# Performance work log

Measured on AMD Instinct MI355X. Metric: run time of the kernel, lower is better.

Reference implementation:

```python
import jax, jax.numpy as jnp
import numpy as np

B, T, C = 2, 2048, 1024
N_HEAD = 16
HEAD_DIM = C // N_HEAD


def setup_inputs() -> dict:
    key = jax.random.key(0)
    k1, k2, k3 = jax.random.split(key, 3)
    s = 1.0 / np.sqrt(C)
    return {
        "x": jax.random.normal(k1, (B, T, C), dtype=jnp.float32),
        "w_qkv": jax.random.normal(k2, (C, 3 * C), dtype=jnp.float32) * s,
        "b_qkv": jnp.zeros((3 * C,), dtype=jnp.float32),
        "w_out": jax.random.normal(k3, (C, C), dtype=jnp.float32) * s,
        "b_out": jnp.zeros((C,), dtype=jnp.float32),
    }


def reference(x, w_qkv, b_qkv, w_out, b_out):
    b, t, c = x.shape
    qkv = x @ w_qkv + b_qkv                                   # [B,T,3C]
    # Faithful to torch: view(B,T,H,3*hd).transpose(1,2) then split last dim
    qkv = qkv.reshape(b, t, N_HEAD, 3 * HEAD_DIM).transpose(0, 2, 1, 3)  # [B,H,T,3hd]
    q, k, v = jnp.split(qkv, 3, axis=-1)                      # each [B,H,T,hd]
    att = jnp.einsum("bhqd,bhkd->bhqk", q, k) / np.sqrt(HEAD_DIM)
    causal = jnp.tril(jnp.ones((t, t), dtype=bool))
    att = jnp.where(causal[None, None], att, -jnp.inf)
    att = jax.nn.softmax(att, axis=-1)                        # dropout p=0 (eval)
    y = jnp.einsum("bhqk,bhkd->bhqd", att, v)                 # [B,H,T,hd]
    y = y.transpose(0, 2, 1, 3).reshape(b, t, c)
    return y @ w_out + b_out
```

## Files before the change

kernel.cpp:

```cpp
#include <hip/hip_runtime.h>


#define T_SEQ 2048
#define C_DIM 1024
#define NH    16
#define HD    64
#define BT    4096

typedef short bf16x8 __attribute__((ext_vector_type(8)));
typedef float floatx4 __attribute__((ext_vector_type(4)));

static __device__ __forceinline__ unsigned short f2bf(float f) {
    union { float f; unsigned u; } v; v.f = f;
    unsigned u = v.u;
    return (unsigned short)((u + 0x7FFFu + ((u >> 16) & 1u)) >> 16);
}
static __device__ __forceinline__ float bf2f(unsigned short u) {
    union { unsigned u; float f; } v; v.u = ((unsigned)u) << 16; return v.f;
}
static __device__ __forceinline__ float exp2_fast(float x) {
    float r; asm("v_exp_f32 %0, %1" : "=v"(r) : "v"(x)); return r;
}
static __device__ __forceinline__ unsigned cvt_pk_bf16(float lo, float hi) {
    unsigned r; asm("v_cvt_pk_bf16_f32 %0, %1, %2" : "=v"(r) : "v"(lo), "v"(hi)); return r;
}

static __device__ __forceinline__ void gl2lds16(const void* g, void* l) {
    __builtin_amdgcn_global_load_lds(
        (const __attribute__((address_space(1))) unsigned int*)g,
        (__attribute__((address_space(3))) unsigned int*)l, 16, 0, 0);
}

static __device__ __forceinline__ void transpose_body(float (*tile)[65],
                                                      const float* __restrict__ W,
                                                      unsigned short* __restrict__ Wt,
                                                      int K, int N, int bx, int by) {
    const int k0 = by << 6;
    const int n0 = bx << 6;
    const int rr = threadIdx.x >> 4;
    const int cc = (threadIdx.x & 15) << 2;
#pragma unroll
    for (int i = 0; i < 4; i++) {
        int r = rr + (i << 4);
        *(float4*)&tile[r][cc] = *(const float4*)(W + (size_t)(k0 + r) * N + n0 + cc);
    }
    __syncthreads();
#pragma unroll
    for (int i = 0; i < 4; i++) {
        int nr = rr + (i << 4);
        ushort4 o;
        o.x = f2bf(tile[cc + 0][nr]);
        o.y = f2bf(tile[cc + 1][nr]);
        o.z = f2bf(tile[cc + 2][nr]);
        o.w = f2bf(tile[cc + 3][nr]);
        *(ushort4*)(Wt + (size_t)(n0 + nr) * K + k0 + cc) = o;
    }
}

__global__ __launch_bounds__(256) void prep(const float* __restrict__ x,
                                            unsigned short* __restrict__ xb,
                                            const float* __restrict__ w_qkv,
                                            unsigned short* __restrict__ wqkvT,
                                            const float* __restrict__ w_out,
                                            unsigned short* __restrict__ woutT) {
    __shared__ float tile[64][65];
    const int bx = blockIdx.x;
    if (bx < 1024) {
        int i = (bx * 256 + threadIdx.x) * 4;
        const int n = BT * C_DIM;
        const int stride = 1024 * 1024;
        for (; i < n; i += stride) {
            float4 f = *(const float4*)(x + i);
            ushort4 o;
            o.x = f2bf(f.x); o.y = f2bf(f.y); o.z = f2bf(f.z); o.w = f2bf(f.w);
            *(ushort4*)(xb + i) = o;
        }
    } else if (bx < 1024 + 768) {
        int b = bx - 1024;
        transpose_body(tile, w_qkv, wqkvT, 1024, 3072, b % 48, b / 48);
    } else {
        int b = bx - 1024 - 768;
        transpose_body(tile, w_out, woutT, 1024, 1024, b % 16, b / 16);
    }
}

__global__ __launch_bounds__(256) void transp_v(const unsigned short* __restrict__ vb,
                                                unsigned short* __restrict__ vt) {
    __shared__ unsigned short tile[64][68];
    const int t0 = blockIdx.x << 6;
    const int bh = blockIdx.y;
    const size_t base = (size_t)bh * T_SEQ * HD;
    const int r = threadIdx.x >> 3;
    const int c = (threadIdx.x & 7) << 3;
#pragma unroll
    for (int i = 0; i < 2; i++) {
        const unsigned short* src = vb + base + (size_t)(t0 + r + (i << 5)) * HD + c;
        ushort4 u0 = *(const ushort4*)src;
        ushort4 u1 = *(const ushort4*)(src + 4);
        *(ushort4*)&tile[r + (i << 5)][c] = u0;
        *(ushort4*)&tile[r + (i << 5)][c + 4] = u1;
    }
    __syncthreads();
#pragma unroll
    for (int i = 0; i < 2; i++) {
        int s = threadIdx.x + (i << 8);
        int d = s >> 3;
        int tc = (s & 7) << 3;
        ushort4 o0, o1;
        o0.x = tile[tc + 0][d]; o0.y = tile[tc + 1][d];
        o0.z = tile[tc + 2][d]; o0.w = tile[tc + 3][d];
        o1.x = tile[tc + 4][d]; o1.y = tile[tc + 5][d];
        o1.z = tile[tc + 6][d]; o1.w = tile[tc + 7][d];
        unsigned short* dst = vt + ((size_t)bh * HD + d) * T_SEQ + t0 + tc;
        *(ushort4*)dst = o0;
        *(ushort4*)(dst + 4) = o1;
    }
}

#define GEMM_CORE(A_, Bt_, K_)                                                      \
    __shared__ short As[128 * 64];                                                  \
    __shared__ short Bs[128 * 64];                                                  \
    const int tid  = threadIdx.x;                                                   \
    const int lane = tid & 63, wave = tid >> 6;                                     \
    const int ln   = lane & 15, quad = lane >> 4;                                   \
    const int wm   = wave & 1,  wn   = wave >> 1;                                   \
    const int row0 = blockIdx.y << 7;                                               \
    const int col0 = blockIdx.x << 7;                                               \
    floatx4 acc[4][4];                                                              \
    _Pragma("unroll")                                                               \
    for (int i = 0; i < 4; i++)                                                     \
        _Pragma("unroll")                                                           \
        for (int j = 0; j < 4; j++) acc[i][j] = (floatx4){0.f, 0.f, 0.f, 0.f};      \
    for (int k0 = 0; k0 < K_; k0 += 64) {                                           \
        _Pragma("unroll")                                                           \
        for (int i = 0; i < 4; i++) {                                               \
            int c = (i << 8) + tid;                                                 \
            int r = c >> 3;                                                         \
            int gsrc = (c & 7) ^ (r & 7);                                           \
            gl2lds16(A_  + (size_t)(row0 + r) * K_ + k0 + (gsrc << 3), &As[c << 3]); \
            gl2lds16(Bt_ + (size_t)(col0 + r) * K_ + k0 + (gsrc << 3), &Bs[c << 3]); \
        }                                                                           \
        __syncthreads();                                                            \
        _Pragma("unroll")                                                           \
        for (int half = 0; half < 2; half++) {                                      \
            bf16x8 af[4], bfr[4];                                                   \
            _Pragma("unroll")                                                       \
            for (int t4 = 0; t4 < 4; t4++) {                                        \
                int ra = (wm << 6) + (t4 << 4) + ln;                                \
                int rb = (wn << 6) + (t4 << 4) + ln;                                \
                int g  = (half << 2) + quad;                                        \
                af[t4]  = *(bf16x8*)&As[((ra << 3) + (g ^ (ra & 7))) << 3];         \
                bfr[t4] = *(bf16x8*)&Bs[((rb << 3) + (g ^ (rb & 7))) << 3];         \
            }                                                                       \
            _Pragma("unroll")                                                       \
            for (int mt = 0; mt < 4; mt++)                                          \
                _Pragma("unroll")                                                   \
                for (int nt = 0; nt < 4; nt++)                                      \
                    acc[mt][nt] = __builtin_amdgcn_mfma_f32_16x16x32_bf16(af[mt], bfr[nt], acc[mt][nt], 0, 0, 0); \
        }                                                                           \
        __syncthreads();                                                            \
    }

__global__ __launch_bounds__(256) void gemm_qkv(const unsigned short* __restrict__ A,
                                                const unsigned short* __restrict__ Bt,
                                                const float* __restrict__ bias,
                                                unsigned short* __restrict__ qb,
                                                unsigned short* __restrict__ kb,
                                                unsigned short* __restrict__ vb) {
    GEMM_CORE(A, Bt, 1024)
    const float QSCALE = 0.125f * 1.4426950408889634f;
#pragma unroll
    for (int mt = 0; mt < 4; mt++) {
#pragma unroll
        for (int nt = 0; nt < 4; nt++) {
            int n = col0 + (wn << 6) + (nt << 4) + ln;
            int h = n / 192, r = n % 192;
            int sel = r >> 6, d = r & 63;
            float bv = bias[n];
#pragma unroll
            for (int e = 0; e < 4; e++) {
                int m = row0 + (wm << 6) + (mt << 4) + (quad << 2) + e;
                int b = m >> 11, t = m & 2047;
                float val = acc[mt][nt][e] + bv;
                size_t idx = (((size_t)(b * NH + h)) * T_SEQ + t) * HD + d;
                if (sel == 0)
                    qb[idx] = f2bf(val * QSCALE);
                else if (sel == 1)
                    kb[idx] = f2bf(val);
                else
                    vb[idx] = f2bf(val);
            }
        }
    }
}

__global__ __launch_bounds__(256) void gemm_out(const unsigned short* __restrict__ A,
                                                const unsigned short* __restrict__ Bt,
                                                const float* __restrict__ bias,
                                                float* __restrict__ out) {
    const int K = 1024, N = 1024;
    __shared__ short As[128 * 64];
    __shared__ short Bs[64 * 64];
    const int tid  = threadIdx.x;
    const int lane = tid & 63, wave = tid >> 6;
    const int ln   = lane & 15, quad = lane >> 4;
    const int wm   = wave & 1,  wn   = wave >> 1;
    const int row0 = blockIdx.y << 7;
    const int col0 = blockIdx.x << 6;
    floatx4 acc[4][2];
#pragma unroll
    for (int i = 0; i < 4; i++)
#pragma unroll
        for (int j = 0; j < 2; j++) acc[i][j] = (floatx4){0.f, 0.f, 0.f, 0.f};
    for (int k0 = 0; k0 < K; k0 += 64) {
#pragma unroll
        for (int i = 0; i < 4; i++) {
            int c = (i << 8) + tid;
            int r = c >> 3;
            int gsrc = (c & 7) ^ (r & 7);
            gl2lds16(A + (size_t)(row0 + r) * K + k0 + (gsrc << 3), &As[c << 3]);
        }
#pragma unroll
        for (int i = 0; i < 2; i++) {
            int c = (i << 8) + tid;
            int r = c >> 3;
            int gsrc = (c & 7) ^ (r & 7);
            gl2lds16(Bt + (size_t)(col0 + r) * K + k0 + (gsrc << 3), &Bs[c << 3]);
        }
        __syncthreads();
#pragma unroll
        for (int half = 0; half < 2; half++) {
            bf16x8 af[4], bfr[2];
#pragma unroll
            for (int t4 = 0; t4 < 4; t4++) {
                int ra = (wm << 6) + (t4 << 4) + ln;
                int g  = (half << 2) + quad;
                af[t4] = *(bf16x8*)&As[((ra << 3) + (g ^ (ra & 7))) << 3];
            }
#pragma unroll
            for (int t2 = 0; t2 < 2; t2++) {
                int rb = (wn << 5) + (t2 << 4) + ln;
                int g  = (half << 2) + quad;
                bfr[t2] = *(bf16x8*)&Bs[((rb << 3) + (g ^ (rb & 7))) << 3];
            }
#pragma unroll
            for (int mt = 0; mt < 4; mt++)
#pragma unroll
                for (int nt = 0; nt < 2; nt++)
                    acc[mt][nt] = __builtin_amdgcn_mfma_f32_16x16x32_bf16(af[mt], bfr[nt], acc[mt][nt], 0, 0, 0);
        }
        __syncthreads();
    }
#pragma unroll
    for (int mt = 0; mt < 4; mt++) {
#pragma unroll
        for (int nt = 0; nt < 2; nt++) {
            int n = col0 + (wn << 5) + (nt << 4) + ln;
            float bv = bias[n];
#pragma unroll
            for (int e = 0; e < 4; e++) {
                int m = row0 + (wm << 6) + (mt << 4) + (quad << 2) + e;
                out[(size_t)m * N + n] = acc[mt][nt][e] + bv;
            }
        }
    }
}

__global__ __launch_bounds__(256, 4) void attn_p1(const unsigned short* __restrict__ qb,
                                                  const unsigned short* __restrict__ kb,
                                                  const unsigned short* __restrict__ vt,
                                                  unsigned short* __restrict__ y,
                                                  unsigned short* __restrict__ po,
                                                  float* __restrict__ pm,
                                                  float* __restrict__ pl) {
    __shared__ short Ks[64][68];
    __shared__ short Vs[64][68];
    __shared__ short QP[64][68];
    const int tid  = threadIdx.x;
    const int w    = tid >> 6, lane = tid & 63;
    const int ln   = lane & 15, quad = lane >> 4;
    const int bx   = blockIdx.x;
    int qt, c;
    if (bx < 32)      { qt = 31 - bx;        c = 0; }
    else if (bx < 56) { qt = 31 - (bx - 32); c = 1; }
    else if (bx < 72) { qt = 31 - (bx - 56); c = 2; }
    else              { qt = 31 - (bx - 72); c = 3; }
    const int kt_lo = c << 3;
    const int kt_hi = (kt_lo + 7 < qt) ? (kt_lo + 7) : qt;
    const int nc    = (qt >> 3) + 1;
    const bool fin  = (nc == 1);
    const int bh   = blockIdx.y;
    const size_t base = (size_t)bh * T_SEQ * HD;
    const int q0   = qt << 6;
    const int sb   = q0 + (w << 4);
    const float NEG_INF = -__builtin_inff();

    const int sr = tid >> 3;
    const int sc = (tid & 7) << 3;

    const unsigned short* qrow = qb + base + (size_t)(q0 + (w << 4) + ln) * HD;
    bf16x8 bq0 = *(const bf16x8*)(qrow + (quad << 3));
    bf16x8 bq1 = *(const bf16x8*)(qrow + 32 + (quad << 3));

    bf16x8 kreg[2], vreg[2];
    const int kk0 = kt_lo << 6;
#pragma unroll
    for (int i = 0; i < 2; i++) {
        kreg[i] = *(const bf16x8*)(kb + base + (size_t)(kk0 + sr + (i << 5)) * HD + sc);
        vreg[i] = *(const bf16x8*)(vt + base + (size_t)(sr + (i << 5)) * T_SEQ + kk0 + sc);
    }

    floatx4 o[4];
#pragma unroll
    for (int nt = 0; nt < 4; nt++) o[nt] = (floatx4){0.f, 0.f, 0.f, 0.f};
    float m_prev = NEG_INF, l_run = 0.f;

    for (int kt = kt_lo; kt <= kt_hi; kt++) {
        const int k0 = kt << 6;
        __syncthreads();
#pragma unroll
        for (int i = 0; i < 2; i++) {
            *(bf16x8*)&Ks[sr + (i << 5)][sc] = kreg[i];
            *(bf16x8*)&Vs[sr + (i << 5)][sc] = vreg[i];
        }
        __syncthreads();
        if (kt < kt_hi) {
            const int kn = k0 + 64;
#pragma unroll
            for (int i = 0; i < 2; i++) {
                kreg[i] = *(const bf16x8*)(kb + base + (size_t)(kn + sr + (i << 5)) * HD + sc);
                vreg[i] = *(const bf16x8*)(vt + base + (size_t)(sr + (i << 5)) * T_SEQ + kn + sc);
            }
        }

        const bool diag  = (kt == qt);
        const int  nlive = diag ? w : 3;

        floatx4 st[4];
        __builtin_amdgcn_s_setprio(1);
#pragma unroll
        for (int ktl = 0; ktl < 4; ktl++) {
            if (ktl <= nlive) {
                bf16x8 a0 = *(bf16x8*)&Ks[(ktl << 4) + ln][quad << 3];
                bf16x8 a1 = *(bf16x8*)&Ks[(ktl << 4) + ln][32 + (quad << 3)];
                floatx4 acc = (floatx4){0.f, 0.f, 0.f, 0.f};
                acc = __builtin_amdgcn_mfma_f32_16x16x32_bf16(a0, bq0, acc, 0, 0, 0);
                acc = __builtin_amdgcn_mfma_f32_16x16x32_bf16(a1, bq1, acc, 0, 0, 0);
                st[ktl] = acc;
            }
        }
        __builtin_amdgcn_s_setprio(0);
        if (diag) {
#pragma unroll
            for (int ktl = 0; ktl < 4; ktl++) {
                if (ktl <= nlive) {
#pragma unroll
                    for (int e = 0; e < 4; e++) {
                        int kg = k0 + (ktl << 4) + (quad << 2) + e;
                        if (kg > sb + ln) st[ktl][e] = NEG_INF;
                    }
                }
            }
        }

        float mx = NEG_INF;
#pragma unroll
        for (int ktl = 0; ktl < 4; ktl++)
            if (ktl <= nlive) {
                mx = fmaxf(mx, fmaxf(fmaxf(st[ktl][0], st[ktl][1]),
                                     fmaxf(st[ktl][2], st[ktl][3])));
            }
        mx = fmaxf(mx, __shfl_xor(mx, 16));
        mx = fmaxf(mx, __shfl_xor(mx, 32));
        const bool need = __any(mx > m_prev);
        const float m_new = fmaxf(m_prev, mx);
        float psum = 0.f;
#pragma unroll
        for (int ktl = 0; ktl < 4; ktl++)
            if (ktl <= nlive) {
#pragma unroll
                for (int e = 0; e < 4; e++) {
                    float p = exp2_fast(st[ktl][e] - m_new);
                    st[ktl][e] = p;
                    psum += p;
                }
            }
        psum += __shfl_xor(psum, 16);
        psum += __shfl_xor(psum, 32);

#pragma unroll
        for (int ktl = 0; ktl < 4; ktl++) {
            uint2 pw;
            if (ktl <= nlive) {
                pw.x = cvt_pk_bf16(st[ktl][0], st[ktl][1]);
                pw.y = cvt_pk_bf16(st[ktl][2], st[ktl][3]);
            } else {
                pw.x = 0; pw.y = 0;
            }
            *(uint2*)&QP[(w << 4) + ln][(ktl << 4) + (quad << 2)] = pw;
        }

        if (need) {
            float alpha = exp2_fast(m_prev - m_new);
            float arow[4];
#pragma unroll
            for (int e = 0; e < 4; e++) arow[e] = __shfl(alpha, (quad << 2) + e);
#pragma unroll
            for (int nt = 0; nt < 4; nt++)
#pragma unroll
                for (int e = 0; e < 4; e++) o[nt][e] *= arow[e];
            l_run = l_run * alpha + psum;
            m_prev = m_new;
        } else {
            l_run += psum;
        }

        bf16x8 ap0 = *(bf16x8*)&QP[(w << 4) + ln][quad << 3];
        bf16x8 ap1 = *(bf16x8*)&QP[(w << 4) + ln][32 + (quad << 3)];
        __builtin_amdgcn_s_setprio(1);
#pragma unroll
        for (int nt = 0; nt < 4; nt++) {
            bf16x8 v0 = *(bf16x8*)&Vs[(nt << 4) + ln][quad << 3];
            bf16x8 v1 = *(bf16x8*)&Vs[(nt << 4) + ln][32 + (quad << 3)];
            o[nt] = __builtin_amdgcn_mfma_f32_16x16x32_bf16(ap0, v0, o[nt], 0, 0, 0);
            o[nt] = __builtin_amdgcn_mfma_f32_16x16x32_bf16(ap1, v1, o[nt], 0, 0, 0);
        }
        __builtin_amdgcn_s_setprio(0);
    }

    if (fin) {
        float linv[4];
#pragma unroll
        for (int e = 0; e < 4; e++) linv[e] = 1.0f / __shfl(l_run, (quad << 2) + e);
        const int b = bh >> 4, h = bh & 15;
#pragma unroll
        for (int e = 0; e < 4; e++) {
            int t = sb + (quad << 2) + e;
            unsigned short* yrow = y + ((size_t)b * T_SEQ + t) * C_DIM + h * HD;
#pragma unroll
            for (int nt = 0; nt < 4; nt++)
                yrow[(nt << 4) + ln] = f2bf(o[nt][e] * linv[e]);
        }
    } else {
        int cb;
        if (qt < 16)      cb = (qt - 8) * 2;
        else if (qt < 24) cb = 16 + (qt - 16) * 3;
        else              cb = 40 + (qt - 24) * 4;
        const int slot = bh * 72 + cb + c;
        if (quad == 0) {
            pm[(slot << 6) + (w << 4) + ln] = m_prev;
            pl[(slot << 6) + (w << 4) + ln] = l_run;
        }
#pragma unroll
        for (int e = 0; e < 4; e++) {
            int q = (w << 4) + (quad << 2) + e;
            unsigned short* porow = po + (((size_t)slot << 6) + q) * HD;
#pragma unroll
            for (int nt = 0; nt < 4; nt++)
                porow[(nt << 4) + ln] = f2bf(o[nt][e]);
        }
    }
}

__global__ __launch_bounds__(256) void attn_p2(const unsigned short* __restrict__ po,
                                               const float* __restrict__ pm,
                                               const float* __restrict__ pl,
                                               unsigned short* __restrict__ y) {
    const int qt = 8 + blockIdx.x;
    const int bh = blockIdx.y;
    const int nc = (qt >> 3) + 1;
    int cb;
    if (qt < 16)      cb = (qt - 8) * 2;
    else if (qt < 24) cb = 16 + (qt - 16) * 3;
    else              cb = 40 + (qt - 24) * 4;
    const int slot0 = bh * 72 + cb;
    const int tid = threadIdx.x;
    const int q  = tid >> 2;
    const int d0 = (tid & 3) << 4;
    const float NEG_INF = -__builtin_inff();

    float mv[4], lv[4];
#pragma unroll
    for (int cc = 0; cc < 4; cc++) {
        if (cc < nc) {
            mv[cc] = pm[((slot0 + cc) << 6) + q];
            lv[cc] = pl[((slot0 + cc) << 6) + q];
        } else {
            mv[cc] = NEG_INF; lv[cc] = 0.f;
        }
    }
    float m = fmaxf(fmaxf(mv[0], mv[1]), fmaxf(mv[2], mv[3]));
    float a[4];
    float L = 0.f;
#pragma unroll
    for (int cc = 0; cc < 4; cc++) {
        a[cc] = (cc < nc) ? exp2_fast(mv[cc] - m) : 0.f;
        L += lv[cc] * a[cc];
    }
    const float inv = 1.0f / L;
#pragma unroll
    for (int cc = 0; cc < 4; cc++) a[cc] *= inv;

    float acc[16];
#pragma unroll
    for (int i = 0; i < 16; i++) acc[i] = 0.f;
#pragma unroll
    for (int cc = 0; cc < 4; cc++) {
        if (cc < nc) {
            const unsigned short* r = po + (((size_t)(slot0 + cc)) << 12) + (q << 6) + d0;
            const float ac = a[cc];
#pragma unroll
            for (int i = 0; i < 4; i++) {
                ushort4 u = *(const ushort4*)(r + (i << 2));
                acc[(i << 2) + 0] += ac * bf2f(u.x);
                acc[(i << 2) + 1] += ac * bf2f(u.y);
                acc[(i << 2) + 2] += ac * bf2f(u.z);
                acc[(i << 2) + 3] += ac * bf2f(u.w);
            }
        }
    }

    const int b = bh >> 4, h = bh & 15;
    const int t = (qt << 6) + q;
    unsigned short* yrow = y + ((size_t)b * T_SEQ + t) * C_DIM + h * HD + d0;
#pragma unroll
    for (int i = 0; i < 4; i++) {
        ushort4 ow;
        ow.x = f2bf(acc[(i << 2) + 0]);
        ow.y = f2bf(acc[(i << 2) + 1]);
        ow.z = f2bf(acc[(i << 2) + 2]);
        ow.w = f2bf(acc[(i << 2) + 3]);
        *(ushort4*)(yrow + (i << 2)) = ow;
    }
}

extern "C" void kernel_launch(void* const* d_in, const int* in_sizes, int n_in,
                              void* d_out, int out_size, void* d_ws, size_t ws_size,
                              hipStream_t stream) {
    (void)in_sizes; (void)n_in; (void)out_size; (void)ws_size;
    const float* x     = (const float*)d_in[0];
    const float* w_qkv = (const float*)d_in[1];
    const float* b_qkv = (const float*)d_in[2];
    const float* w_out = (const float*)d_in[3];
    const float* b_out = (const float*)d_in[4];
    float* out = (float*)d_out;

    char* ws = (char*)d_ws;
    unsigned short* qb    = (unsigned short*)ws;
    unsigned short* kb    = (unsigned short*)(ws + ((size_t)8  << 20));
    unsigned short* vt    = (unsigned short*)(ws + ((size_t)16 << 20));
    unsigned short* xb    = (unsigned short*)(ws + ((size_t)24 << 20));
    unsigned short* yb    = xb;
    unsigned short* woutT = (unsigned short*)(ws + ((size_t)32 << 20));
    unsigned short* vb    = (unsigned short*)(ws + ((size_t)34 << 20));
    unsigned short* wqkvT = (unsigned short*)(ws + ((size_t)42 << 20));
    unsigned short* po    = (unsigned short*)(ws + ((size_t)34 << 20));
    float*          pm    = (float*)(ws + ((size_t)52 << 20));
    float*          pl    = (float*)(ws + ((size_t)52 << 20) + (640 << 10));

    prep    <<<2048, 256, 0, stream>>>(x, xb, w_qkv, wqkvT, w_out, woutT);
    gemm_qkv<<<dim3(24, 32), 256, 0, stream>>>(xb, wqkvT, b_qkv, qb, kb, vb);
    transp_v<<<dim3(32, 32), 256, 0, stream>>>(vb, vt);
    attn_p1 <<<dim3(80, 32), 256, 0, stream>>>(qb, kb, vt, yb, po, pm, pl);
    attn_p2 <<<dim3(24, 32), 256, 0, stream>>>(po, pm, pl, yb);
    gemm_out<<<dim3(16, 32), 256, 0, stream>>>(yb, woutT, b_out, out);
}
```

Baseline: 204.7 us.

## Read K/V directly from global memory and remap blocks so heads share an XCD

```diff
diff --git a/kernel.cpp b/kernel.cpp
--- a/kernel.cpp
+++ b/kernel.cpp
@@ -266,20 +266,24 @@
     }
 }
 
-__global__ __launch_bounds__(256, 4) void attn_p1(const unsigned short* __restrict__ qb,
-                                                  const unsigned short* __restrict__ kb,
-                                                  const unsigned short* __restrict__ vt,
-                                                  unsigned short* __restrict__ y,
-                                                  unsigned short* __restrict__ po,
-                                                  float* __restrict__ pm,
-                                                  float* __restrict__ pl) {
-    __shared__ short Ks[64][68];
-    __shared__ short Vs[64][68];
+__global__ __launch_bounds__(256) void attn_p1(const unsigned short* __restrict__ qb,
+                                               const unsigned short* __restrict__ kb,
+                                               const unsigned short* __restrict__ vt,
+                                               unsigned short* __restrict__ y,
+                                               unsigned short* __restrict__ po,
+                                               float* __restrict__ pm,
+                                               float* __restrict__ pl) {
     __shared__ short QP[64][68];
     const int tid  = threadIdx.x;
     const int w    = tid >> 6, lane = tid & 63;
     const int ln   = lane & 15, quad = lane >> 4;
-    const int bx   = blockIdx.x;
+
+    const int L     = blockIdx.y * 80 + blockIdx.x;
+    const int xcd   = L & 7;
+    const int slotL = L >> 3;
+    const int bh    = xcd + ((slotL / 80) << 3);
+    const int bx    = slotL % 80;
+
     int qt, c;
     if (bx < 32)      { qt = 31 - bx;        c = 0; }
     else if (bx < 56) { qt = 31 - (bx - 32); c = 1; }
@@ -289,27 +293,15 @@
     const int kt_hi = (kt_lo + 7 < qt) ? (kt_lo + 7) : qt;
     const int nc    = (qt >> 3) + 1;
     const bool fin  = (nc == 1);
-    const int bh   = blockIdx.y;
     const size_t base = (size_t)bh * T_SEQ * HD;
     const int q0   = qt << 6;
     const int sb   = q0 + (w << 4);
     const float NEG_INF = -__builtin_inff();
 
-    const int sr = tid >> 3;
-    const int sc = (tid & 7) << 3;
-
     const unsigned short* qrow = qb + base + (size_t)(q0 + (w << 4) + ln) * HD;
     bf16x8 bq0 = *(const bf16x8*)(qrow + (quad << 3));
     bf16x8 bq1 = *(const bf16x8*)(qrow + 32 + (quad << 3));
 
-    bf16x8 kreg[2], vreg[2];
-    const int kk0 = kt_lo << 6;
-#pragma unroll
-    for (int i = 0; i < 2; i++) {
-        kreg[i] = *(const bf16x8*)(kb + base + (size_t)(kk0 + sr + (i << 5)) * HD + sc);
-        vreg[i] = *(const bf16x8*)(vt + base + (size_t)(sr + (i << 5)) * T_SEQ + kk0 + sc);
-    }
-
     floatx4 o[4];
 #pragma unroll
     for (int nt = 0; nt < 4; nt++) o[nt] = (floatx4){0.f, 0.f, 0.f, 0.f};
@@ -317,22 +309,6 @@
 
     for (int kt = kt_lo; kt <= kt_hi; kt++) {
         const int k0 = kt << 6;
-        __syncthreads();
-#pragma unroll
-        for (int i = 0; i < 2; i++) {
-            *(bf16x8*)&Ks[sr + (i << 5)][sc] = kreg[i];
-            *(bf16x8*)&Vs[sr + (i << 5)][sc] = vreg[i];
-        }
-        __syncthreads();
-        if (kt < kt_hi) {
-            const int kn = k0 + 64;
-#pragma unroll
-            for (int i = 0; i < 2; i++) {
-                kreg[i] = *(const bf16x8*)(kb + base + (size_t)(kn + sr + (i << 5)) * HD + sc);
-                vreg[i] = *(const bf16x8*)(vt + base + (size_t)(sr + (i << 5)) * T_SEQ + kn + sc);
-            }
-        }
-
         const bool diag  = (kt == qt);
         const int  nlive = diag ? w : 3;
 
@@ -341,8 +317,10 @@
 #pragma unroll
         for (int ktl = 0; ktl < 4; ktl++) {
             if (ktl <= nlive) {
-                bf16x8 a0 = *(bf16x8*)&Ks[(ktl << 4) + ln][quad << 3];
-                bf16x8 a1 = *(bf16x8*)&Ks[(ktl << 4) + ln][32 + (quad << 3)];
+                const unsigned short* krow =
+                    kb + base + (size_t)(k0 + (ktl << 4) + ln) * HD + (quad << 3);
+                bf16x8 a0 = *(const bf16x8*)krow;
+                bf16x8 a1 = *(const bf16x8*)(krow + 32);
                 floatx4 acc = (floatx4){0.f, 0.f, 0.f, 0.f};
                 acc = __builtin_amdgcn_mfma_f32_16x16x32_bf16(a0, bq0, acc, 0, 0, 0);
                 acc = __builtin_amdgcn_mfma_f32_16x16x32_bf16(a1, bq1, acc, 0, 0, 0);
@@ -420,8 +398,10 @@
         __builtin_amdgcn_s_setprio(1);
 #pragma unroll
         for (int nt = 0; nt < 4; nt++) {
-            bf16x8 v0 = *(bf16x8*)&Vs[(nt << 4) + ln][quad << 3];
-            bf16x8 v1 = *(bf16x8*)&Vs[(nt << 4) + ln][32 + (quad << 3)];
+            const unsigned short* vrow =
+                vt + base + (size_t)((nt << 4) + ln) * T_SEQ + k0 + (quad << 3);
+            bf16x8 v0 = *(const bf16x8*)vrow;
+            bf16x8 v1 = *(const bf16x8*)(vrow + 32);
             o[nt] = __builtin_amdgcn_mfma_f32_16x16x32_bf16(ap0, v0, o[nt], 0, 0, 0);
             o[nt] = __builtin_amdgcn_mfma_f32_16x16x32_bf16(ap1, v1, o[nt], 0, 0, 0);
         }
```

Result: slower. 310.3 us (+51.5%).

## Double-buffer K/V tiles in attention and remap blocks for XCD locality

Applied to the files above, without the earlier changes.

```diff
diff --git a/kernel.cpp b/kernel.cpp
--- a/kernel.cpp
+++ b/kernel.cpp
@@ -266,20 +266,26 @@
     }
 }
 
-__global__ __launch_bounds__(256, 4) void attn_p1(const unsigned short* __restrict__ qb,
-                                                  const unsigned short* __restrict__ kb,
-                                                  const unsigned short* __restrict__ vt,
-                                                  unsigned short* __restrict__ y,
-                                                  unsigned short* __restrict__ po,
-                                                  float* __restrict__ pm,
-                                                  float* __restrict__ pl) {
-    __shared__ short Ks[64][68];
-    __shared__ short Vs[64][68];
+__global__ __launch_bounds__(256) void attn_p1(const unsigned short* __restrict__ qb,
+                                               const unsigned short* __restrict__ kb,
+                                               const unsigned short* __restrict__ vt,
+                                               unsigned short* __restrict__ y,
+                                               unsigned short* __restrict__ po,
+                                               float* __restrict__ pm,
+                                               float* __restrict__ pl) {
+    __shared__ short Ks[2][64][68];
+    __shared__ short Vs[2][64][68];
     __shared__ short QP[64][68];
     const int tid  = threadIdx.x;
     const int w    = tid >> 6, lane = tid & 63;
     const int ln   = lane & 15, quad = lane >> 4;
-    const int bx   = blockIdx.x;
+
+    const int L     = blockIdx.y * 80 + blockIdx.x;
+    const int xcd   = L & 7;
+    const int slotL = L >> 3;
+    const int bh    = xcd + ((slotL / 80) << 3);
+    const int bx    = slotL % 80;
+
     int qt, c;
     if (bx < 32)      { qt = 31 - bx;        c = 0; }
     else if (bx < 56) { qt = 31 - (bx - 32); c = 1; }
@@ -289,7 +295,6 @@
     const int kt_hi = (kt_lo + 7 < qt) ? (kt_lo + 7) : qt;
     const int nc    = (qt >> 3) + 1;
     const bool fin  = (nc == 1);
-    const int bh   = blockIdx.y;
     const size_t base = (size_t)bh * T_SEQ * HD;
     const int q0   = qt << 6;
     const int sb   = q0 + (w << 4);
@@ -309,6 +314,12 @@
         kreg[i] = *(const bf16x8*)(kb + base + (size_t)(kk0 + sr + (i << 5)) * HD + sc);
         vreg[i] = *(const bf16x8*)(vt + base + (size_t)(sr + (i << 5)) * T_SEQ + kk0 + sc);
     }
+#pragma unroll
+    for (int i = 0; i < 2; i++) {
+        *(bf16x8*)&Ks[0][sr + (i << 5)][sc] = kreg[i];
+        *(bf16x8*)&Vs[0][sr + (i << 5)][sc] = vreg[i];
+    }
+    int cur = 0;
 
     floatx4 o[4];
 #pragma unroll
@@ -318,12 +329,6 @@
     for (int kt = kt_lo; kt <= kt_hi; kt++) {
         const int k0 = kt << 6;
         __syncthreads();
-#pragma unroll
-        for (int i = 0; i < 2; i++) {
-            *(bf16x8*)&Ks[sr + (i << 5)][sc] = kreg[i];
-            *(bf16x8*)&Vs[sr + (i << 5)][sc] = vreg[i];
-        }
-        __syncthreads();
         if (kt < kt_hi) {
             const int kn = k0 + 64;
 #pragma unroll
@@ -341,8 +346,8 @@
 #pragma unroll
         for (int ktl = 0; ktl < 4; ktl++) {
             if (ktl <= nlive) {
-                bf16x8 a0 = *(bf16x8*)&Ks[(ktl << 4) + ln][quad << 3];
-                bf16x8 a1 = *(bf16x8*)&Ks[(ktl << 4) + ln][32 + (quad << 3)];
+                bf16x8 a0 = *(bf16x8*)&Ks[cur][(ktl << 4) + ln][quad << 3];
+                bf16x8 a1 = *(bf16x8*)&Ks[cur][(ktl << 4) + ln][32 + (quad << 3)];
                 floatx4 acc = (floatx4){0.f, 0.f, 0.f, 0.f};
                 acc = __builtin_amdgcn_mfma_f32_16x16x32_bf16(a0, bq0, acc, 0, 0, 0);
                 acc = __builtin_amdgcn_mfma_f32_16x16x32_bf16(a1, bq1, acc, 0, 0, 0);
@@ -420,12 +425,21 @@
         __builtin_amdgcn_s_setprio(1);
 #pragma unroll
         for (int nt = 0; nt < 4; nt++) {
-            bf16x8 v0 = *(bf16x8*)&Vs[(nt << 4) + ln][quad << 3];
-            bf16x8 v1 = *(bf16x8*)&Vs[(nt << 4) + ln][32 + (quad << 3)];
+            bf16x8 v0 = *(bf16x8*)&Vs[cur][(nt << 4) + ln][quad << 3];
+            bf16x8 v1 = *(bf16x8*)&Vs[cur][(nt << 4) + ln][32 + (quad << 3)];
             o[nt] = __builtin_amdgcn_mfma_f32_16x16x32_bf16(ap0, v0, o[nt], 0, 0, 0);
             o[nt] = __builtin_amdgcn_mfma_f32_16x16x32_bf16(ap1, v1, o[nt], 0, 0, 0);
         }
         __builtin_amdgcn_s_setprio(0);
+
+        if (kt < kt_hi) {
+#pragma unroll
+            for (int i = 0; i < 2; i++) {
+                *(bf16x8*)&Ks[cur ^ 1][sr + (i << 5)][sc] = kreg[i];
+                *(bf16x8*)&Vs[cur ^ 1][sr + (i << 5)][sc] = vreg[i];
+            }
+        }
+        cur ^= 1;
     }
 
     if (fin) {
```

Measured after the change: 212.2 us. +3.6%, slower.

## Fuse V transpose into QKV GEMM epilogue and remap attention blocks to XCDs

Applied to the files above, without the earlier changes.

```diff
diff --git a/kernel.cpp b/kernel.cpp
--- a/kernel.cpp
+++ b/kernel.cpp
@@ -81,39 +81,6 @@
     } else {
         int b = bx - 1024 - 768;
         transpose_body(tile, w_out, woutT, 1024, 1024, b % 16, b / 16);
-    }
-}
-
-__global__ __launch_bounds__(256) void transp_v(const unsigned short* __restrict__ vb,
-                                                unsigned short* __restrict__ vt) {
-    __shared__ unsigned short tile[64][68];
-    const int t0 = blockIdx.x << 6;
-    const int bh = blockIdx.y;
-    const size_t base = (size_t)bh * T_SEQ * HD;
-    const int r = threadIdx.x >> 3;
-    const int c = (threadIdx.x & 7) << 3;
-#pragma unroll
-    for (int i = 0; i < 2; i++) {
-        const unsigned short* src = vb + base + (size_t)(t0 + r + (i << 5)) * HD + c;
-        ushort4 u0 = *(const ushort4*)src;
-        ushort4 u1 = *(const ushort4*)(src + 4);
-        *(ushort4*)&tile[r + (i << 5)][c] = u0;
-        *(ushort4*)&tile[r + (i << 5)][c + 4] = u1;
-    }
-    __syncthreads();
-#pragma unroll
-    for (int i = 0; i < 2; i++) {
-        int s = threadIdx.x + (i << 8);
-        int d = s >> 3;
-        int tc = (s & 7) << 3;
-        ushort4 o0, o1;
-        o0.x = tile[tc + 0][d]; o0.y = tile[tc + 1][d];
-        o0.z = tile[tc + 2][d]; o0.w = tile[tc + 3][d];
-        o1.x = tile[tc + 4][d]; o1.y = tile[tc + 5][d];
-        o1.z = tile[tc + 6][d]; o1.w = tile[tc + 7][d];
-        unsigned short* dst = vt + ((size_t)bh * HD + d) * T_SEQ + t0 + tc;
-        *(ushort4*)dst = o0;
-        *(ushort4*)(dst + 4) = o1;
     }
 }
 
@@ -166,7 +133,7 @@
                                                 const float* __restrict__ bias,
                                                 unsigned short* __restrict__ qb,
                                                 unsigned short* __restrict__ kb,
-                                                unsigned short* __restrict__ vb) {
+                                                unsigned short* __restrict__ vt) {
     GEMM_CORE(A, Bt, 1024)
     const float QSCALE = 0.125f * 1.4426950408889634f;
 #pragma unroll
@@ -177,18 +144,27 @@
             int h = n / 192, r = n % 192;
             int sel = r >> 6, d = r & 63;
             float bv = bias[n];
-#pragma unroll
-            for (int e = 0; e < 4; e++) {
-                int m = row0 + (wm << 6) + (mt << 4) + (quad << 2) + e;
-                int b = m >> 11, t = m & 2047;
-                float val = acc[mt][nt][e] + bv;
-                size_t idx = (((size_t)(b * NH + h)) * T_SEQ + t) * HD + d;
-                if (sel == 0)
-                    qb[idx] = f2bf(val * QSCALE);
-                else if (sel == 1)
-                    kb[idx] = f2bf(val);
-                else
-                    vb[idx] = f2bf(val);
+            int m0 = row0 + (wm << 6) + (mt << 4) + (quad << 2);
+            int b  = m0 >> 11, t0 = m0 & 2047;
+            if (sel == 2) {
+                ushort4 o4;
+                o4.x = f2bf(acc[mt][nt][0] + bv);
+                o4.y = f2bf(acc[mt][nt][1] + bv);
+                o4.z = f2bf(acc[mt][nt][2] + bv);
+                o4.w = f2bf(acc[mt][nt][3] + bv);
+                *(ushort4*)(vt + (((size_t)(b * NH + h)) * HD + d) * T_SEQ + t0) = o4;
+            } else if (sel == 0) {
+#pragma unroll
+                for (int e = 0; e < 4; e++) {
+                    size_t idx = (((size_t)(b * NH + h)) * T_SEQ + t0 + e) * HD + d;
+                    qb[idx] = f2bf((acc[mt][nt][e] + bv) * QSCALE);
+                }
+            } else {
+#pragma unroll
+                for (int e = 0; e < 4; e++) {
+                    size_t idx = (((size_t)(b * NH + h)) * T_SEQ + t0 + e) * HD + d;
+                    kb[idx] = f2bf(acc[mt][nt][e] + bv);
+                }
             }
         }
     }
@@ -279,7 +255,13 @@
     const int tid  = threadIdx.x;
     const int w    = tid >> 6, lane = tid & 63;
     const int ln   = lane & 15, quad = lane >> 4;
-    const int bx   = blockIdx.x;
+
+    const int L     = blockIdx.y * 80 + blockIdx.x;
+    const int xcd   = L & 7;
+    const int slotL = L >> 3;
+    const int bh    = xcd + ((slotL / 80) << 3);
+    const int bx    = slotL % 80;
+
     int qt, c;
     if (bx < 32)      { qt = 31 - bx;        c = 0; }
     else if (bx < 56) { qt = 31 - (bx - 32); c = 1; }
@@ -289,7 +271,6 @@
     const int kt_hi = (kt_lo + 7 < qt) ? (kt_lo + 7) : qt;
     const int nc    = (qt >> 3) + 1;
     const bool fin  = (nc == 1);
-    const int bh   = blockIdx.y;
     const size_t base = (size_t)bh * T_SEQ * HD;
     const int q0   = qt << 6;
     const int sb   = q0 + (w << 4);
@@ -552,15 +533,13 @@
     unsigned short* xb    = (unsigned short*)(ws + ((size_t)24 << 20));
     unsigned short* yb    = xb;
     unsigned short* woutT = (unsigned short*)(ws + ((size_t)32 << 20));
-    unsigned short* vb    = (unsigned short*)(ws + ((size_t)34 << 20));
     unsigned short* wqkvT = (unsigned short*)(ws + ((size_t)42 << 20));
     unsigned short* po    = (unsigned short*)(ws + ((size_t)34 << 20));
     float*          pm    = (float*)(ws + ((size_t)52 << 20));
     float*          pl    = (float*)(ws + ((size_t)52 << 20) + (640 << 10));
 
     prep    <<<2048, 256, 0, stream>>>(x, xb, w_qkv, wqkvT, w_out, woutT);
-    gemm_qkv<<<dim3(24, 32), 256, 0, stream>>>(xb, wqkvT, b_qkv, qb, kb, vb);
-    transp_v<<<dim3(32, 32), 256, 0, stream>>>(vb, vt);
+    gemm_qkv<<<dim3(24, 32), 256, 0, stream>>>(xb, wqkvT, b_qkv, qb, kb, vt);
     attn_p1 <<<dim3(80, 32), 256, 0, stream>>>(qb, kb, vt, yb, po, pm, pl);
     attn_p2 <<<dim3(24, 32), 256, 0, stream>>>(po, pm, pl, yb);
     gemm_out<<<dim3(16, 32), 256, 0, stream>>>(yb, woutT, b_out, out);
```

Result: faster. 197.2 us (-3.7%).
